# Performance work log

Hardware: AMD Instinct MI355X
Metric: run time of the kernel (lower is better)

## Reference

```python
import jax, jax.numpy as jnp
import numpy as np

B, S, D, H = 2, 2048, 1024, 16
HD = D // H  # head dim = 64


def setup_inputs() -> dict:
    key = jax.random.key(0)
    k0, k1, k2 = jax.random.split(key, 3)
    x = jax.random.normal(k0, (B, S, D), dtype=jnp.float32)
    # fused QKV projection: nn.Linear(D, 3D) -> weight [3D, D], bias [3D]
    Wqkv_w = jax.random.normal(k1, (3 * D, D), dtype=jnp.float32) * (1.0 / np.sqrt(D))
    Wqkv_b = jnp.zeros((3 * D,), dtype=jnp.float32)
    out_w = jax.random.normal(k2, (D, D), dtype=jnp.float32) * (1.0 / np.sqrt(D))
    out_b = jnp.zeros((D,), dtype=jnp.float32)
    # ALiBi-like additive bias, shape [1, H, 1, S] (broadcasts over queries)
    slopes = 2.0 ** (-8.0 * jnp.arange(1, H + 1, dtype=jnp.float32) / H)  # [H]
    dist = (S - 1) - jnp.arange(S, dtype=jnp.float32)                      # [S]
    attn_bias = (-slopes[:, None] * dist[None, :]).reshape(1, H, 1, S)
    # key padding mask: second sequence is padded by 256 tokens at the end
    lengths = jnp.array([S, S - 256])
    attention_mask = jnp.arange(S)[None, :] < lengths[:, None]             # [B, S] bool
    return {"x": x, "Wqkv_w": Wqkv_w, "Wqkv_b": Wqkv_b, "out_w": out_w,
            "out_b": out_b, "attn_bias": attn_bias, "attention_mask": attention_mask}


def reference(x, Wqkv_w, Wqkv_b, out_w, out_b, attn_bias, attention_mask):
    b, s, d = x.shape
    # fused QKV projection, then chunk into q, k, v along feature dim
    qkv = jnp.einsum('bsd,ed->bse', x, Wqkv_w) + Wqkv_b  # [b, s, 3d]
    q, k, v = jnp.split(qkv, 3, axis=-1)
    # b s (h hd) -> b h s hd
    q = q.reshape(b, s, H, HD).transpose(0, 2, 1, 3)
    k = k.reshape(b, s, H, HD).transpose(0, 2, 1, 3)
    v = v.reshape(b, s, H, HD).transpose(0, 2, 1, 3)
    softmax_scale = 1.0 / np.sqrt(HD)
    aw = jnp.einsum('bhqe,bhke->bhqk', q, k) * softmax_scale  # [b, H, s, s]
    aw = aw + attn_bias  # attn_bias broadcasts [1,H,1,s] -> [b,H,s,s]
    min_val = jnp.finfo(aw.dtype).min
    # key padding mask: mask positions where attention_mask is False
    aw = jnp.where(attention_mask[:, None, None, :], aw, min_val)
    # causal mask (is_causal=True, s_q == s_k)
    causal = jnp.tril(jnp.ones((s, s), dtype=bool))
    aw = jnp.where(causal[None, None, :, :], aw, min_val)
    p = jax.nn.softmax(aw, axis=-1)
    out = jnp.einsum('bhqk,bhke->bhqe', p, v)  # [b, H, s, HD]
    out = out.transpose(0, 2, 1, 3).reshape(b, s, d)
    return jnp.einsum('bsd,ed->bse', out, out_w) + out_b
```

## Files before the change

### kernel.cpp

```cpp
#include <hip/hip_runtime.h>
#include <hip/hip_bf16.h>
#include <stdint.h>

typedef __attribute__((ext_vector_type(8))) short s16x8;
typedef __attribute__((ext_vector_type(8))) unsigned short u16x8;
typedef __attribute__((ext_vector_type(4))) float f32x4;

#define SEQ 2048
#define LOG2E 1.44269504088896f

__device__ __forceinline__ unsigned short f2b(float x) {
  union { __hip_bfloat16 h; unsigned short u; } cv;
  cv.h = __float2bfloat16(x);
  return cv.u;
}

__device__ __forceinline__ float exp2fast(float x) {
  float r;
  asm("v_exp_f32 %0, %1" : "=v"(r) : "v"(x));
  return r;
}

__device__ __forceinline__ void gload16(const void* g, void* l) {
  __builtin_amdgcn_global_load_lds(
      (const __attribute__((address_space(1))) void*)g,
      (__attribute__((address_space(3))) void*)l, 16, 0, 0);
}

__global__ void cvt_all(const float* __restrict__ x, const float* __restrict__ wq,
                        const float* __restrict__ ow, const float* __restrict__ abias,
                        const void* __restrict__ maskp,
                        __hip_bfloat16* __restrict__ xb, __hip_bfloat16* __restrict__ wqb,
                        __hip_bfloat16* __restrict__ owb, float* __restrict__ biasm) {
  const int i = blockIdx.x * 256 + threadIdx.x;
  if (i >= 2097152) {
    const int j = i - 2097152;
    const int b = j >> 15, h = (j >> 11) & 15, kv = j & 2047;
    const int* mi = (const int*)maskp;
    const unsigned char* mb = (const unsigned char*)maskp;
    const bool int_fmt = (mi[0] == 0 || mi[0] == 1);
    const bool ok = int_fmt ? (mi[b * SEQ + kv] != 0) : (mb[b * SEQ + kv] != 0);
    biasm[j] = ok ? abias[h * SEQ + kv] * LOG2E : -1e30f;
    return;
  }
  const float* src;
  __hip_bfloat16* dst;
  int off;
  if (i < 1048576) { src = x; dst = xb; off = i; }
  else if (i < 1835008) { src = wq; dst = wqb; off = i - 1048576; }
  else { src = ow; dst = owb; off = i - 1835008; }
  float4 v = reinterpret_cast<const float4*>(src)[off];
  ushort4 o;
  o.x = f2b(v.x); o.y = f2b(v.y); o.z = f2b(v.z); o.w = f2b(v.w);
  reinterpret_cast<ushort4*>(dst)[off] = o;
}

template <int MODE, int BM>
__global__ __launch_bounds__(256) void gemm_bt(
    const __hip_bfloat16* __restrict__ A, const __hip_bfloat16* __restrict__ B,
    const float* __restrict__ bias, void* __restrict__ Cout,
    __hip_bfloat16* __restrict__ Vt, int M, int N, int K) {
  constexpr int MR = BM / 32;
  __shared__ __align__(16) __hip_bfloat16 As[BM * 32];
  __shared__ __align__(16) __hip_bfloat16 Bs[128 * 32];
  const int tid = threadIdx.x;
  const int lane = tid & 63;
  const int w = tid >> 6;
  const int wr = w >> 1, wc = w & 1;
  const int rowg = blockIdx.x * BM;
  const int colg = blockIdx.y * 128;
  const int lr = lane & 15;
  const int lk = (lane >> 4) * 8;
  f32x4 acc[MR][4];
#pragma unroll
  for (int m = 0; m < MR; ++m)
#pragma unroll
    for (int n = 0; n < 4; ++n) acc[m][n] = (f32x4){0.f, 0.f, 0.f, 0.f};
  for (int kt = 0; kt < K; kt += 32) {
#pragma unroll
    for (int r = 0; r < BM / 64; ++r) {
      const int idx = r * 256 + tid;
      gload16(A + (size_t)(rowg + (idx >> 2)) * K + kt + (idx & 3) * 8, As + idx * 8);
    }
#pragma unroll
    for (int r = 0; r < 2; ++r) {
      const int idx = r * 256 + tid;
      gload16(B + (size_t)(colg + (idx >> 2)) * K + kt + (idx & 3) * 8, Bs + idx * 8);
    }
    __syncthreads();
    s16x8 af[MR], bfr[4];
#pragma unroll
    for (int m = 0; m < MR; ++m)
      af[m] = *reinterpret_cast<const s16x8*>(As + (wr * (BM / 2) + m * 16 + lr) * 32 + lk);
#pragma unroll
    for (int n = 0; n < 4; ++n)
      bfr[n] = *reinterpret_cast<const s16x8*>(Bs + (wc * 64 + n * 16 + lr) * 32 + lk);
#pragma unroll
    for (int m = 0; m < MR; ++m)
#pragma unroll
      for (int n = 0; n < 4; ++n)
        acc[m][n] = __builtin_amdgcn_mfma_f32_16x16x32_bf16(af[m], bfr[n], acc[m][n], 0, 0, 0);
    __syncthreads();
  }
  const int r0l = (lane >> 4) * 4;
#pragma unroll
  for (int m = 0; m < MR; ++m) {
#pragma unroll
    for (int n = 0; n < 4; ++n) {
      const int col = colg + wc * 64 + n * 16 + lr;
      const int row0 = rowg + wr * (BM / 2) + m * 16 + r0l;
      const float bv = bias[col];
      if (MODE == 0) {
        __hip_bfloat16* qkb = (__hip_bfloat16*)Cout;
        if (col < 1024) {
#pragma unroll
          for (int j = 0; j < 4; ++j)
            qkb[(size_t)(row0 + j) * 2048 + col] = __float2bfloat16(acc[m][n][j] + bv);
        } else if (col < 2048) {
          const int dd = col & 63;
          const int base = col - dd;
#pragma unroll
          for (int j = 0; j < 4; ++j) {
            const int s = row0 + j;
            qkb[(size_t)s * 2048 + base + (dd ^ ((s & 7) << 3))] =
                __float2bfloat16(acc[m][n][j] + bv);
          }
        } else {
          const int c2 = col - 2048;
          const int dd = c2 & 63;
          const int bb = row0 >> 11;
          const int s0 = (row0 & 2047) ^ ((dd & 7) << 3);
          ushort4 pk;
          unsigned short* pp = (unsigned short*)&pk;
#pragma unroll
          for (int j = 0; j < 4; ++j) pp[j] = f2b(acc[m][n][j] + bv);
          *reinterpret_cast<ushort4*>(
              Vt + ((size_t)(bb * 16 + (c2 >> 6)) * 64 + dd) * 2048 + s0) = pk;
        }
      } else {
        float* o = (float*)Cout;
#pragma unroll
        for (int j = 0; j < 4; ++j)
          o[(size_t)(row0 + j) * N + col] = acc[m][n][j] + bv;
      }
    }
  }
}

__device__ __forceinline__ void attn_tile(
    const char* Ks, const char* Vs, char* pw, const float* bmb,
    s16x8 aq0, s16x8 aq1, int lane, int kv0, int q_abs, bool causal,
    int rd0, int rd1, const int* pwo,
    float m_r, float& l_r, f32x4* oa) {
  const int g = lane >> 4;
  const float SCALE2 = 0.125f * LOG2E;
  f32x4 bvp[4];
#pragma unroll
  for (int n = 0; n < 4; ++n) {
    bvp[n] = *reinterpret_cast<const f32x4*>(bmb + kv0 + n * 16 + g * 4);
#pragma unroll
    for (int j = 0; j < 4; ++j) bvp[n][j] -= m_r;
  }
  f32x4 sf[4];
  __builtin_amdgcn_s_setprio(1);
#pragma unroll
  for (int n = 0; n < 4; ++n) {
    s16x8 ak0 = *reinterpret_cast<const s16x8*>(Ks + rd0 + n * 2048);
    s16x8 ak1 = *reinterpret_cast<const s16x8*>(Ks + rd1 + n * 2048);
    f32x4 z = (f32x4){0.f, 0.f, 0.f, 0.f};
    z = __builtin_amdgcn_mfma_f32_16x16x32_bf16(ak0, aq0, z, 0, 0, 0);
    z = __builtin_amdgcn_mfma_f32_16x16x32_bf16(ak1, aq1, z, 0, 0, 0);
    sf[n] = z;
  }
  __builtin_amdgcn_s_setprio(0);
#pragma unroll
  for (int n = 0; n < 4; ++n)
#pragma unroll
    for (int j = 0; j < 4; ++j) sf[n][j] = fmaf(sf[n][j], SCALE2, bvp[n][j]);
  if (causal) {
    const int kvb = kv0 + g * 4;
#pragma unroll
    for (int n = 0; n < 4; ++n)
#pragma unroll
      for (int j = 0; j < 4; ++j)
        if (kvb + n * 16 + j > q_abs) sf[n][j] = -1e30f;
  }
  float ps[4];
#pragma unroll
  for (int n = 0; n < 4; ++n) {
#pragma unroll
    for (int j = 0; j < 4; ++j) sf[n][j] = exp2fast(sf[n][j]);
    ps[n] = (sf[n][0] + sf[n][1]) + (sf[n][2] + sf[n][3]);
  }
  l_r += (ps[0] + ps[1]) + (ps[2] + ps[3]);
  s16x8 bva[4], bvb[4];
#pragma unroll
  for (int d = 0; d < 4; ++d) {
    bva[d] = *reinterpret_cast<const s16x8*>(Vs + rd0 + d * 2048);
    bvb[d] = *reinterpret_cast<const s16x8*>(Vs + rd1 + d * 2048);
  }
#pragma unroll
  for (int n = 0; n < 4; ++n) {
    union { ushort4 u; uint2 v; } pk;
    pk.u.x = f2b(sf[n][0]); pk.u.y = f2b(sf[n][1]);
    pk.u.z = f2b(sf[n][2]); pk.u.w = f2b(sf[n][3]);
    *reinterpret_cast<uint2*>(pw + pwo[n]) = pk.v;
  }
  s16x8 pa0 = *reinterpret_cast<const s16x8*>(pw + rd0);
  s16x8 pa1 = *reinterpret_cast<const s16x8*>(pw + rd1);
  __builtin_amdgcn_s_setprio(1);
#pragma unroll
  for (int d = 0; d < 4; ++d) {
    oa[d] = __builtin_amdgcn_mfma_f32_16x16x32_bf16(pa0, bva[d], oa[d], 0, 0, 0);
    oa[d] = __builtin_amdgcn_mfma_f32_16x16x32_bf16(pa1, bvb[d], oa[d], 0, 0, 0);
  }
  __builtin_amdgcn_s_setprio(0);
}

__global__ __launch_bounds__(512, 4) void attn_fwd6(
    const __hip_bfloat16* __restrict__ qk, const __hip_bfloat16* __restrict__ Vt,
    const float* __restrict__ biasm, __hip_bfloat16* __restrict__ O) {
  __shared__ __align__(16) char KV[2][2][2][8192];
  __shared__ __align__(16) char Ps[8][2048];
  const int tid = threadIdx.x;
  const int lane = tid & 63;
  const int w = tid >> 6;
  const int wsub = w & 3;
  const int z = w >> 2;
  const int bid = blockIdx.x;
  const int qt = 31 - (bid >> 5);
  const int bh = bid & 31;
  const int b = bh >> 4, h = bh & 15;
  const int row0 = qt * 64 + wsub * 16;
  const int lr = lane & 15;
  const int g = lane >> 4;
  const int NTit = (qt >> 1) + 1;
  const int xm = (lr & 7) << 4;
  const int lkB = g * 16;
  const int rd0 = lr * 128 + (lkB ^ xm);
  const int rd1 = lr * 128 + ((64 + lkB) ^ xm);
  const int pwo[4] = {lr * 128 + ((g * 8) ^ xm),       lr * 128 + ((32 + g * 8) ^ xm),
                      lr * 128 + ((64 + g * 8) ^ xm),  lr * 128 + ((96 + g * 8) ^ xm)};
  const __hip_bfloat16* qptr =
      qk + (size_t)(b * SEQ + row0 + lr) * 2048 + h * 64 + g * 8;
  const s16x8 aq0 = *reinterpret_cast<const s16x8*>(qptr);
  const s16x8 aq1 = *reinterpret_cast<const s16x8*>(qptr + 32);
  const int q_abs = row0 + lr;
  const float* bmb = biasm + (size_t)bh * 2048;
  float mb = bmb[q_abs];
  if (mb < -1e29f) {
    int lo = 0, hi = q_abs;
    while (lo < hi) {
      const int mid = (lo + hi + 1) >> 1;
      if (bmb[mid] < -1e29f) hi = mid - 1; else lo = mid;
    }
    mb = bmb[lo];
  }
  const float m_r = mb + 12.0f;
  float l_r = 0.f;
  f32x4 oa[4];
#pragma unroll
  for (int d = 0; d < 4; ++d) oa[d] = (f32x4){0.f, 0.f, 0.f, 0.f};
  const int r_ = tid >> 3;
  const int c16 = tid & 7;
  const __hip_bfloat16* kb = qk + ((size_t)b * SEQ + r_) * 2048 + 1024 + h * 64 + c16 * 8;
  const __hip_bfloat16* vb = Vt + ((size_t)bh * 64 + r_) * 2048 + c16 * 8;
#define ISSUE(T, C)                                                     \
  {                                                                     \
    const int tE_ = 2 * (T);                                            \
    const int tO_ = (2 * (T) + 1 <= qt) ? (2 * (T) + 1) : qt;           \
    gload16(kb + (size_t)(tE_ * 64) * 2048, KV[0][C][0] + tid * 16);    \
    gload16(kb + (size_t)(tO_ * 64) * 2048, KV[1][C][0] + tid * 16);    \
    gload16(vb + tE_ * 64, KV[0][C][1] + tid * 16);                     \
    gload16(vb + tO_ * 64, KV[1][C][1] + tid * 16);                     \
  }
  ISSUE(0, 0);
  __syncthreads();
  int cur = 0;
  for (int t = 0; t < NTit; ++t) {
    if (t + 1 < NTit) ISSUE(t + 1, cur ^ 1);
    const int tz = 2 * t + z;
    if (tz <= qt)
      attn_tile(KV[z][cur][0], KV[z][cur][1], Ps[w], bmb, aq0, aq1, lane,
                tz * 64, q_abs, tz == qt, rd0, rd1, pwo, m_r, l_r, oa);
    __syncthreads();
    cur ^= 1;
  }
#undef ISSUE
  l_r += __shfl_xor(l_r, 16);
  l_r += __shfl_xor(l_r, 32);
  float* mlbuf = (float*)&KV[0][0][0][0];
  if (z == 1) {
    float* mo = (float*)(&Ps[0][0] + wsub * 4096);
#pragma unroll
    for (int d = 0; d < 4; ++d)
#pragma unroll
      for (int j = 0; j < 4; ++j)
        mo[(g * 4 + j) * 64 + d * 16 + lr] = oa[d][j];
    if (lane < 16) {
      mlbuf[wsub * 32 + lr] = m_r;
      mlbuf[wsub * 32 + 16 + lr] = l_r;
    }
  }
  __syncthreads();
  if (z == 0) {
    const float mB = mlbuf[wsub * 32 + lr];
    const float lB = mlbuf[wsub * 32 + 16 + lr];
    const float mS = fmaxf(m_r, mB);
    const float fA = exp2fast(m_r - mS);
    const float fB = exp2fast(mB - mS);
    const float linv = 1.0f / (l_r * fA + lB * fB);
    float fAj[4], fBj[4], lij[4];
#pragma unroll
    for (int j = 0; j < 4; ++j) {
      fAj[j] = __shfl(fA, g * 4 + j);
      fBj[j] = __shfl(fB, g * 4 + j);
      lij[j] = __shfl(linv, g * 4 + j);
    }
    const float* mo = (const float*)(&Ps[0][0] + wsub * 4096);
#pragma unroll
    for (int d = 0; d < 4; ++d)
#pragma unroll
      for (int j = 0; j < 4; ++j) {
        const float v =
            (oa[d][j] * fAj[j] + mo[(g * 4 + j) * 64 + d * 16 + lr] * fBj[j]) * lij[j];
        O[(size_t)(b * SEQ + row0 + g * 4 + j) * 1024 + h * 64 + d * 16 + lr] =
            __float2bfloat16(v);
      }
  }
}

extern "C" void kernel_launch(void* const* d_in, const int* in_sizes, int n_in,
                              void* d_out, int out_size, void* d_ws, size_t ws_size,
                              hipStream_t stream) {
  const float* x     = (const float*)d_in[0];
  const float* wqkv  = (const float*)d_in[1];
  const float* bqkv  = (const float*)d_in[2];
  const float* wout  = (const float*)d_in[3];
  const float* bout  = (const float*)d_in[4];
  const float* abias = (const float*)d_in[5];
  const void*  mask  = d_in[6];

  __hip_bfloat16* ws  = (__hip_bfloat16*)d_ws;
  __hip_bfloat16* xb  = ws;
  __hip_bfloat16* wqb = ws + 4194304;
  __hip_bfloat16* owb = ws + 7340032;
  __hip_bfloat16* qkb = ws + 8388608;
  __hip_bfloat16* vtb = ws + 16777216;
  float*          bmf = (float*)(ws + 20971520);
  __hip_bfloat16* aob = xb;

  cvt_all<<<8448, 256, 0, stream>>>(x, wqkv, wout, abias, mask, xb, wqb, owb, bmf);
  gemm_bt<0, 128><<<dim3(32, 24), 256, 0, stream>>>(xb, wqb, bqkv, (void*)qkb, vtb,
                                                    4096, 3072, 1024);
  attn_fwd6<<<1024, 512, 0, stream>>>(qkb, vtb, bmf, aob);
  gemm_bt<1, 64><<<dim3(64, 8), 256, 0, stream>>>(aob, owb, bout, d_out,
                                                  (__hip_bfloat16*)nullptr, 4096, 1024, 1024);
}
```

Before: 114.0 us.

## Double-buffer GEMM LDS tiles to overlap global loads with MFMA

Splits the A/B shared-memory tiles into two buffers and prefetches the next K-slice into the alternate buffer while the current one feeds the MFMAs. This leaves one barrier per K iteration instead of two and aims to hide global-load latency behind compute. Bias values are also loaded once per column before the epilogue. LDS usage doubles, which may reduce occupancy.

```diff
diff --git a/kernel.cpp b/kernel.cpp
--- a/kernel.cpp
+++ b/kernel.cpp
@@ -61,8 +61,8 @@
     const float* __restrict__ bias, void* __restrict__ Cout,
     __hip_bfloat16* __restrict__ Vt, int M, int N, int K) {
   constexpr int MR = BM / 32;
-  __shared__ __align__(16) __hip_bfloat16 As[BM * 32];
-  __shared__ __align__(16) __hip_bfloat16 Bs[128 * 32];
+  __shared__ __align__(16) __hip_bfloat16 As[2][BM * 32];
+  __shared__ __align__(16) __hip_bfloat16 Bs[2][128 * 32];
   const int tid = threadIdx.x;
   const int lane = tid & 63;
   const int w = tid >> 6;
@@ -76,40 +76,53 @@
   for (int m = 0; m < MR; ++m)
 #pragma unroll
     for (int n = 0; n < 4; ++n) acc[m][n] = (f32x4){0.f, 0.f, 0.f, 0.f};
+#define GSTAGE(KT, C)                                                            \
+  {                                                                              \
+    _Pragma("unroll") for (int r = 0; r < BM / 64; ++r) {                        \
+      const int idx = r * 256 + tid;                                             \
+      gload16(A + (size_t)(rowg + (idx >> 2)) * K + (KT) + (idx & 3) * 8,        \
+              &As[C][0] + idx * 8);                                              \
+    }                                                                            \
+    _Pragma("unroll") for (int r = 0; r < 2; ++r) {                              \
+      const int idx = r * 256 + tid;                                             \
+      gload16(B + (size_t)(colg + (idx >> 2)) * K + (KT) + (idx & 3) * 8,        \
+              &Bs[C][0] + idx * 8);                                              \
+    }                                                                            \
+  }
+  GSTAGE(0, 0);
+  __syncthreads();
+  int cur = 0;
   for (int kt = 0; kt < K; kt += 32) {
-#pragma unroll
-    for (int r = 0; r < BM / 64; ++r) {
-      const int idx = r * 256 + tid;
-      gload16(A + (size_t)(rowg + (idx >> 2)) * K + kt + (idx & 3) * 8, As + idx * 8);
-    }
-#pragma unroll
-    for (int r = 0; r < 2; ++r) {
-      const int idx = r * 256 + tid;
-      gload16(B + (size_t)(colg + (idx >> 2)) * K + kt + (idx & 3) * 8, Bs + idx * 8);
-    }
-    __syncthreads();
+    if (kt + 32 < K) GSTAGE(kt + 32, cur ^ 1);
     s16x8 af[MR], bfr[4];
 #pragma unroll
     for (int m = 0; m < MR; ++m)
-      af[m] = *reinterpret_cast<const s16x8*>(As + (wr * (BM / 2) + m * 16 + lr) * 32 + lk);
+      af[m] = *reinterpret_cast<const s16x8*>(&As[cur][0] +
+                                              (wr * (BM / 2) + m * 16 + lr) * 32 + lk);
 #pragma unroll
     for (int n = 0; n < 4; ++n)
-      bfr[n] = *reinterpret_cast<const s16x8*>(Bs + (wc * 64 + n * 16 + lr) * 32 + lk);
+      bfr[n] = *reinterpret_cast<const s16x8*>(&Bs[cur][0] +
+                                               (wc * 64 + n * 16 + lr) * 32 + lk);
 #pragma unroll
     for (int m = 0; m < MR; ++m)
 #pragma unroll
       for (int n = 0; n < 4; ++n)
         acc[m][n] = __builtin_amdgcn_mfma_f32_16x16x32_bf16(af[m], bfr[n], acc[m][n], 0, 0, 0);
     __syncthreads();
-  }
+    cur ^= 1;
+  }
+#undef GSTAGE
   const int r0l = (lane >> 4) * 4;
+  float bvn[4];
+#pragma unroll
+  for (int n = 0; n < 4; ++n) bvn[n] = bias[colg + wc * 64 + n * 16 + lr];
 #pragma unroll
   for (int m = 0; m < MR; ++m) {
 #pragma unroll
     for (int n = 0; n < 4; ++n) {
       const int col = colg + wc * 64 + n * 16 + lr;
       const int row0 = rowg + wr * (BM / 2) + m * 16 + r0l;
-      const float bv = bias[col];
+      const float bv = bvn[n];
       if (MODE == 0) {
         __hip_bfloat16* qkb = (__hip_bfloat16*)Cout;
         if (col < 1024) {
```

After: 108.0 us, median of 2. -5.3%, faster.
